# Kernel optimization log

Hardware: AMD Instinct MI355X
Metric: run time of the kernel (lower is better)

Reference implementation:

```python
import jax, jax.numpy as jnp
import numpy as np

B, S, D, H = 2, 2048, 1024, 16
HD = D // H  # head_dim = 64
ROPE_BASE = 10000.0
NEG_MIN = jnp.finfo(jnp.float32).min


def _rope_cos_sin(seq_len, head_dim):
    inv_freq = 1.0 / (ROPE_BASE ** (jnp.arange(0, head_dim, 2, dtype=jnp.float32) / head_dim))
    t = jnp.arange(seq_len, dtype=jnp.float32)
    freqs = jnp.einsum('i,j->ij', t, inv_freq)           # [S, HD/2]
    emb = jnp.concatenate([freqs, freqs], axis=-1)        # [S, HD]
    return jnp.cos(emb), jnp.sin(emb)


def _rotate_half(x):
    x1, x2 = jnp.split(x, 2, axis=-1)
    return jnp.concatenate([-x2, x1], axis=-1)


def setup_inputs() -> dict:
    key = jax.random.key(0)
    ks = jax.random.split(key, 5)
    sc = 0.02
    hidden_states = jax.random.normal(ks[0], (B, S, D), dtype=jnp.float32)
    wq = jax.random.normal(ks[1], (D, D), dtype=jnp.float32) * sc
    wk = jax.random.normal(ks[2], (D, D), dtype=jnp.float32) * sc
    wv = jax.random.normal(ks[3], (D, D), dtype=jnp.float32) * sc
    wo = jax.random.normal(ks[4], (D, D), dtype=jnp.float32) * sc
    # additive causal mask [B,1,S,S]: 0 on/below diagonal, large negative above
    causal = jnp.tril(jnp.ones((S, S), dtype=jnp.bool_))
    attention_mask = jnp.where(causal, 0.0, NEG_MIN)[None, None, :, :].astype(jnp.float32)
    attention_mask = jnp.broadcast_to(attention_mask, (B, 1, S, S))
    position_ids = jnp.broadcast_to(jnp.arange(S, dtype=jnp.int32)[None, :], (B, S))
    return {"hidden_states": hidden_states, "attention_mask": attention_mask,
            "wq": wq, "wk": wk, "wv": wv, "wo": wo, "position_ids": position_ids}


def reference(hidden_states, attention_mask, wq, wk, wv, wo, position_ids):
    bsz, q_len, _ = hidden_states.shape

    def shape_heads(x):
        return x.reshape(bsz, q_len, H, HD).transpose(0, 2, 1, 3)  # [B,H,S,HD]

    q = shape_heads(hidden_states @ wq)
    k = shape_heads(hidden_states @ wk)
    v = shape_heads(hidden_states @ wv)

    cos, sin = _rope_cos_sin(q_len, HD)                   # [S, HD]
    cos = cos[position_ids][:, None, :, :]                # [B,1,S,HD]
    sin = sin[position_ids][:, None, :, :]
    q = q * cos + _rotate_half(q) * sin
    k = k * cos + _rotate_half(k) * sin

    scores = jnp.einsum('bhqd,bhkd->bhqk', q, k) / jnp.sqrt(jnp.float32(HD))
    scores = jnp.maximum(scores + attention_mask, NEG_MIN)
    attn = jax.nn.softmax(scores, axis=-1)
    out = jnp.einsum('bhqk,bhkd->bhqd', attn, v)          # [B,H,S,HD]
    out = out.transpose(0, 2, 1, 3).reshape(bsz, q_len, D)
    return out @ wo
```

## Files before the change

### kernel.cpp

```cpp
#include <hip/hip_runtime.h>
#include <hip/hip_bf16.h>

#define B_ 2
#define S_ 2048
#define D_ 1024
#define H_ 16
#define HD_ 64

typedef unsigned short u16;
typedef __attribute__((ext_vector_type(8))) short short8;
typedef __attribute__((ext_vector_type(4))) float f32x4;

#if __has_builtin(__builtin_amdgcn_exp2f)
#define EXP2F(x) __builtin_amdgcn_exp2f(x)
#else
#define EXP2F(x) exp2f(x)
#endif

__device__ __forceinline__ u16 f2bf(float f) {
  union { float f; unsigned u; } v; v.f = f;
  unsigned r = v.u + 0x7fffu + ((v.u >> 16) & 1u);
  return (u16)(r >> 16);
}
__device__ __forceinline__ unsigned pkbf(float a, float b) {
  union { __hip_bfloat162 h; unsigned u; } v;
  v.h = __float22bfloat162_rn(float2{a, b});
  return v.u;
}
__device__ __forceinline__ void gload_lds16(const u16* g, u16* l) {
  __builtin_amdgcn_global_load_lds((const __attribute__((address_space(1))) void*)g,
                                   (__attribute__((address_space(3))) void*)l, 16, 0, 0);
}

template <int N> struct IC { static constexpr int v = N; };

__global__ __launch_bounds__(256) void prep_kernel(const float* __restrict__ hs,
                                                   const float* __restrict__ W0,
                                                   const float* __restrict__ W1,
                                                   const float* __restrict__ W2,
                                                   const float* __restrict__ W3,
                                                   u16* __restrict__ Xb,
                                                   u16* __restrict__ WT) {
  __shared__ float T[64][65];
  if (blockIdx.z == 4) {
    const int base = (blockIdx.y * 16 + blockIdx.x) * 4096 + threadIdx.x;
#pragma unroll 4
    for (int i = 0; i < 16; ++i) {
      const int idx = base + i * 256;
      const float4 v = ((const float4*)hs)[idx];
      ushort4 o;
      o.x = f2bf(v.x); o.y = f2bf(v.y); o.z = f2bf(v.z); o.w = f2bf(v.w);
      ((ushort4*)Xb)[idx] = o;
    }
    return;
  }
  const float* Wz[4] = {W0, W1, W2, W3};
  const float* W = Wz[blockIdx.z];
  u16* dst = WT + (size_t)blockIdx.z * (1024 * 1024);
  const int nb = blockIdx.x * 64, kb = blockIdx.y * 64;
  const int t = threadIdx.x;
  const int r = t >> 2, c4 = (t & 3) * 16;
#pragma unroll
  for (int i = 0; i < 4; ++i) {
    float4 v = *(const float4*)&W[(kb + r) * D_ + nb + c4 + i * 4];
    T[r][c4 + i * 4 + 0] = v.x;
    T[r][c4 + i * 4 + 1] = v.y;
    T[r][c4 + i * 4 + 2] = v.z;
    T[r][c4 + i * 4 + 3] = v.w;
  }
  __syncthreads();
#pragma unroll
  for (int i = 0; i < 4; ++i) {
    ushort4 o;
    o.x = f2bf(T[c4 + i * 4 + 0][r]);
    o.y = f2bf(T[c4 + i * 4 + 1][r]);
    o.z = f2bf(T[c4 + i * 4 + 2][r]);
    o.w = f2bf(T[c4 + i * 4 + 3][r]);
    *(ushort4*)&dst[(nb + r) * D_ + kb + c4 + i * 4] = o;
  }
}

template <int BN, int MODE>
__global__ __launch_bounds__(256) void gemm_kernel(const u16* __restrict__ A,
                                                   const u16* __restrict__ BT,
                                                   float* __restrict__ out0,
                                                   u16* __restrict__ oQ,
                                                   u16* __restrict__ oK,
                                                   u16* __restrict__ oV,
                                                   const int* __restrict__ posarr) {
  constexpr int K = D_;
  constexpr int BK = 32;
  constexpr int NSTEP = K / BK;
  constexpr int NT = BN / 32;
  constexpr int NBR = (BN * BK) / 2048;
  constexpr int ABANK = 128 * BK;
  constexpr int BBANK = BN * BK;
  constexpr int BUFSZ = ABANK + BBANK;
  constexpr int EPIU = (MODE == 1) ? 128 * 136 : 0;
  constexpr int SMU = (3 * BUFSZ > EPIU) ? 3 * BUFSZ : EPIU;
  __shared__ u16 smem[SMU];

  const int t = threadIdx.x, lane = t & 63, w = t >> 6;
  const int l15 = lane & 15, quad = lane >> 4;
  const int flat = blockIdx.x;
  const int xcd = flat & 7, j = flat >> 3;
  const int m0 = ((xcd << 2) + (j & 3)) * 128;
  const int n0 = (j >> 2) * BN;
  const int wm = (w >> 1) * 64, wn = (w & 1) * (BN / 2);

  f32x4 acc[4][NT];
#pragma unroll
  for (int mt = 0; mt < 4; ++mt)
#pragma unroll
    for (int nt = 0; nt < NT; ++nt) acc[mt][nt] = (f32x4){0.f, 0.f, 0.f, 0.f};

  const u16* agp[2]; int adst[2];
  const u16* bgp[NBR]; int bdst[NBR];
#pragma unroll
  for (int jj = 0; jj < 2; ++jj) {
    const int slot = jj * 256 + w * 64 + lane;
    const int row = slot >> 2, c = slot & 3, q = c ^ ((row >> 1) & 3);
    agp[jj] = A + (size_t)(m0 + row) * K + q * 8;
    adst[jj] = (jj * 256 + w * 64) * 8;
  }
#pragma unroll
  for (int jj = 0; jj < NBR; ++jj) {
    const int slot = jj * 256 + w * 64 + lane;
    const int row = slot >> 2, c = slot & 3, q = c ^ ((row >> 1) & 3);
    bgp[jj] = BT + (size_t)(n0 + row) * K + q * 8;
    bdst[jj] = ABANK + (jj * 256 + w * 64) * 8;
  }

  auto stage = [&](int k0, int buf) {
    u16* base = smem + buf * BUFSZ;
#pragma unroll
    for (int jj = 0; jj < 2; ++jj) gload_lds16(agp[jj] + k0, base + adst[jj]);
#pragma unroll
    for (int jj = 0; jj < NBR; ++jj) gload_lds16(bgp[jj] + k0, base + bdst[jj]);
  };

  int afo[4], bfo[NT];
#pragma unroll
  for (int mt = 0; mt < 4; ++mt) {
    const int row = wm + mt * 16 + l15;
    afo[mt] = row * BK + (quad ^ ((row >> 1) & 3)) * 8;
  }
#pragma unroll
  for (int nt = 0; nt < NT; ++nt) {
    const int col = wn + nt * 16 + l15;
    bfo[nt] = ABANK + col * BK + (quad ^ ((col >> 1) & 3)) * 8;
  }

  auto compute = [&](int buf) {
    const u16* base = smem + buf * BUFSZ;
    short8 af[4], bf[NT];
#pragma unroll
    for (int mt = 0; mt < 4; ++mt) af[mt] = *(const short8*)&base[afo[mt]];
#pragma unroll
    for (int nt = 0; nt < NT; ++nt) bf[nt] = *(const short8*)&base[bfo[nt]];
#pragma unroll
    for (int mt = 0; mt < 4; ++mt)
#pragma unroll
      for (int nt = 0; nt < NT; ++nt)
        acc[mt][nt] = __builtin_amdgcn_mfma_f32_16x16x32_bf16(af[mt], bf[nt], acc[mt][nt], 0, 0, 0);
  };

  stage(0, 0);
  stage(BK, 1);
  int bc = 0, bs = 2;
#pragma unroll 1
  for (int it = 0; it < NSTEP - 2; ++it) {
    if constexpr (MODE == 1) asm volatile("s_waitcnt vmcnt(4)" ::: "memory");
    else                     asm volatile("s_waitcnt vmcnt(3)" ::: "memory");
    __builtin_amdgcn_s_barrier();
    __builtin_amdgcn_sched_barrier(0);
    stage((it + 2) * BK, bs);
    compute(bc);
    bc = bc == 2 ? 0 : bc + 1;
    bs = bs == 2 ? 0 : bs + 1;
  }
  if constexpr (MODE == 1) asm volatile("s_waitcnt vmcnt(4)" ::: "memory");
  else                     asm volatile("s_waitcnt vmcnt(3)" ::: "memory");
  __builtin_amdgcn_s_barrier();
  __builtin_amdgcn_sched_barrier(0);
  compute(bc);
  bc = bc == 2 ? 0 : bc + 1;
  asm volatile("s_waitcnt vmcnt(0)" ::: "memory");
  __builtin_amdgcn_s_barrier();
  __builtin_amdgcn_sched_barrier(0);
  compute(bc);

  if (MODE == 0) {
#pragma unroll
    for (int mt = 0; mt < 4; ++mt) {
      const int row0 = m0 + wm + mt * 16 + quad * 4;
#pragma unroll
      for (int nt = 0; nt < NT; ++nt) {
        const int col = n0 + wn + nt * 16 + l15;
#pragma unroll
        for (int r = 0; r < 4; ++r) out0[(size_t)(row0 + r) * 1024 + col] = acc[mt][nt][r];
      }
    }
  } else {
    const int widx = n0 >> 10;
    if (widx == 2) {
      __syncthreads();
      u16* Epi = smem;
#pragma unroll
      for (int nt = 0; nt < NT; ++nt) {
        const int col = wn + nt * 16 + l15;
#pragma unroll
        for (int mt = 0; mt < 4; ++mt) {
          const int row0 = wm + mt * 16 + quad * 4;
          uint2 pk;
          pk.x = pkbf(acc[mt][nt][0], acc[mt][nt][1]);
          pk.y = pkbf(acc[mt][nt][2], acc[mt][nt][3]);
          *(uint2*)&Epi[col * 136 + row0] = pk;
        }
      }
      __syncthreads();
      const int col = t >> 1, half = t & 1;
      const int cc = (n0 + col) & 1023;
      const int h = cc >> 6, d = cc & 63;
      const int bb = m0 >> 11;
      const int s0 = (m0 & (S_ - 1)) + half * 64;
      u16* gp = oV + ((((size_t)(bb * H_ + h) * HD_ + d)) << 11) + s0;
#pragma unroll
      for (int i = 0; i < 8; ++i)
        ((uint4*)gp)[i] = *(const uint4*)&Epi[col * 136 + half * 64 + i * 8];
    } else {
      u16* dst = (widx == 0) ? oQ : oK;
      const float scale = (widx == 0) ? 0.18033688011f : 1.0f;
      float invf[2];
      invf[0] = exp2f(-0.41524101186f * (float)l15);
      invf[1] = exp2f(-0.41524101186f * (float)(16 + l15));
      __syncthreads();
      u16* Epi = smem;
#pragma unroll
      for (int mt = 0; mt < 4; ++mt) {
        const int lrow0 = wm + mt * 16 + quad * 4;
#pragma unroll
        for (int r = 0; r < 4; ++r) {
          const int rw = m0 + lrow0 + r;
          const int b = rw >> 11, s = rw & (S_ - 1);
          const float pos = (float)posarr[b * S_ + s];
#pragma unroll
          for (int nt2 = 0; nt2 < 2; ++nt2) {
            float sn, c;
            __sincosf(pos * invf[nt2], &sn, &c);
            const float x1 = acc[mt][nt2][r], x2 = acc[mt][nt2 + 2][r];
            const int d = nt2 * 16 + l15;
            Epi[(lrow0 + r) * 136 + wn + d] = f2bf((x1 * c - x2 * sn) * scale);
            Epi[(lrow0 + r) * 136 + wn + d + 32] = f2bf((x2 * c + x1 * sn) * scale);
          }
        }
      }
      __syncthreads();
      const int bb = m0 >> 11, s0 = m0 & (S_ - 1);
      const int sl = t >> 1, d0 = (t & 1) * 32;
#pragma unroll
      for (int hh = 0; hh < 2; ++hh) {
        const int h = ((n0 + hh * 64) & 1023) >> 6;
        u16* gp = dst + (((size_t)(bb * H_ + h) * S_ + s0 + sl) << 6) + d0;
#pragma unroll
        for (int k2 = 0; k2 < 4; ++k2)
          ((uint4*)gp)[k2] = *(const uint4*)&Epi[sl * 136 + hh * 64 + d0 + k2 * 8];
      }
    }
  }
}

__global__ __launch_bounds__(256, 2) void attn_kernel(const u16* __restrict__ Q,
                                                      const u16* __restrict__ Kx,
                                                      const u16* __restrict__ Vt,
                                                      u16* __restrict__ AO) {
  __shared__ u16 Ks[2][2][512 * 8];
  __shared__ u16 Vs[2][2][512 * 8];
  __shared__ u16 Pw[4][2][128 * 8];
  const int t = threadIdx.x;
  const int lane = t & 63, w = t >> 6;
  const int l15 = lane & 15, quad = lane >> 4;
  const int idx = blockIdx.x;
  const int pr = (idx >> 3) & 15;
  const int bh = (idx & 7) | ((idx >> 7) << 3);
  const int qtA = pr, qtB = 31 - pr;
  const u16* qp = Q + bh * (S_ * HD_);
  const u16* kp = Kx + bh * (S_ * HD_);
  const u16* vp = Vt + bh * (HD_ * S_);
  const int wq16 = w * 16;
  const int q_loA = qtA * 64 + wq16;
  const int q_loB = qtB * 64 + wq16;

  int srow[2], sq[2];
#pragma unroll
  for (int jj = 0; jj < 2; ++jj) {
    int slot = w * 128 + jj * 64 + lane;
    srow[jj] = slot >> 3;
    sq[jj] = (slot & 7) ^ (srow[jj] & 7);
  }
  auto stageT = [&](int kt, int buf, int tt) {
#pragma unroll
    for (int jj = 0; jj < 2; ++jj)
      gload_lds16(kp + (size_t)(kt * 64 + srow[jj]) * 64 + sq[jj] * 8,
                  &Ks[buf][tt][(w * 128 + jj * 64) * 8]);
#pragma unroll
    for (int jj = 0; jj < 2; ++jj)
      gload_lds16(vp + (size_t)srow[jj] * S_ + kt * 64 + sq[jj] * 8,
                  &Vs[buf][tt][(w * 128 + jj * 64) * 8]);
  };
  auto stageGroup = [&](int g, int buf, int ktmax) {
    const int kt0 = g * 2;
    stageT(kt0, buf, 0);
    if (kt0 + 1 <= ktmax) stageT(kt0 + 1, buf, 1);
  };

  short8 qfA[2], qfB[2];
#pragma unroll
  for (int kc = 0; kc < 2; ++kc) {
    qfA[kc] = *(const short8*)&qp[(q_loA + l15) * HD_ + kc * 32 + quad * 8];
    qfB[kc] = *(const short8*)&qp[(q_loB + l15) * HD_ + kc * 32 + quad * 8];
  }

  f32x4 oA[4], oB[4];
  f32x4 lsA = (f32x4){0.f, 0.f, 0.f, 0.f}, lsB = (f32x4){0.f, 0.f, 0.f, 0.f};
  float mA = -INFINITY, mB = -INFINITY;
#pragma unroll
  for (int i = 0; i < 4; ++i) {
    oA[i] = (f32x4){0.f, 0.f, 0.f, 0.f};
    oB[i] = (f32x4){0.f, 0.f, 0.f, 0.f};
  }
  const short8 ones = {0x3F80, 0x3F80, 0x3F80, 0x3F80, 0x3F80, 0x3F80, 0x3F80, 0x3F80};

  auto fusedStep = [&](auto NTT, int kt0, int qt_, const short8* qf,
                       f32x4* o, float& m_, f32x4& ls, int buf) {
    constexpr int N2 = decltype(NTT)::v;
    short8 kf[N2][8];
#pragma unroll
    for (int tt = 0; tt < N2; ++tt)
#pragma unroll
      for (int kc = 0; kc < 2; ++kc)
#pragma unroll
        for (int nt = 0; nt < 4; ++nt) {
          const int row = nt * 16 + l15;
          kf[tt][kc * 4 + nt] =
              *(const short8*)&Ks[buf][tt][(row * 8 + ((kc * 4 + quad) ^ (row & 7))) * 8];
        }
    f32x4 sa[N2 * 4];
#pragma unroll
    for (int i = 0; i < N2 * 4; ++i) sa[i] = (f32x4){0.f, 0.f, 0.f, 0.f};
#pragma unroll
    for (int tt = 0; tt < N2; ++tt)
#pragma unroll
      for (int kc = 0; kc < 2; ++kc)
#pragma unroll
        for (int nt = 0; nt < 4; ++nt)
          sa[tt * 4 + nt] = __builtin_amdgcn_mfma_f32_16x16x32_bf16(
              kf[tt][kc * 4 + nt], qf[kc], sa[tt * 4 + nt], 0, 0, 0);
#pragma unroll
    for (int tt = 0; tt < N2; ++tt)
      if (kt0 + tt == qt_) {
#pragma unroll
        for (int nt = 0; nt < 4; ++nt)
#pragma unroll
          for (int r = 0; r < 4; ++r)
            if (nt * 16 + quad * 4 + r > wq16 + l15) sa[tt * 4 + nt][r] = -INFINITY;
      }
    float mx = -INFINITY;
#pragma unroll
    for (int i = 0; i < N2 * 4; ++i)
      mx = fmaxf(mx, fmaxf(fmaxf(sa[i][0], sa[i][1]), fmaxf(sa[i][2], sa[i][3])));
    mx = fmaxf(mx, __shfl_xor(mx, 16));
    mx = fmaxf(mx, __shfl_xor(mx, 32));
    if (!__all(mx <= m_)) {
      const float mn = fmaxf(m_, mx);
      const float alpha = EXP2F(m_ - mn);
      m_ = mn;
#pragma unroll
      for (int dt = 0; dt < 4; ++dt)
#pragma unroll
        for (int r = 0; r < 4; ++r) o[dt][r] *= alpha;
      ls *= alpha;
    }
#pragma unroll
    for (int tt = 0; tt < N2; ++tt)
#pragma unroll
      for (int nt = 0; nt < 4; ++nt) {
        const int q = nt * 2 + (quad >> 1);
        uint2 pk;
        pk.x = pkbf(EXP2F(sa[tt * 4 + nt][0] - m_), EXP2F(sa[tt * 4 + nt][1] - m_));
        pk.y = pkbf(EXP2F(sa[tt * 4 + nt][2] - m_), EXP2F(sa[tt * 4 + nt][3] - m_));
        *(uint2*)&Pw[w][tt][(l15 * 8 + (q ^ (l15 & 7))) * 8 + (quad & 1) * 4] = pk;
      }
    short8 vf[N2][8];
#pragma unroll
    for (int tt = 0; tt < N2; ++tt)
#pragma unroll
      for (int dt = 0; dt < 4; ++dt)
#pragma unroll
        for (int kc = 0; kc < 2; ++kc) {
          const int row = dt * 16 + l15;
          vf[tt][dt * 2 + kc] =
              *(const short8*)&Vs[buf][tt][(row * 8 + ((kc * 4 + quad) ^ (row & 7))) * 8];
        }
#pragma unroll
    for (int tt = 0; tt < N2; ++tt)
#pragma unroll
      for (int kc = 0; kc < 2; ++kc) {
        short8 pf =
            *(const short8*)&Pw[w][tt][(l15 * 8 + (((kc * 4) + quad) ^ (l15 & 7))) * 8];
#pragma unroll
        for (int dt = 0; dt < 4; ++dt)
          o[dt] = __builtin_amdgcn_mfma_f32_16x16x32_bf16(vf[tt][dt * 2 + kc], pf, o[dt], 0, 0, 0);
        ls = __builtin_amdgcn_mfma_f32_16x16x32_bf16(ones, pf, ls, 0, 0, 0);
      }
  };

  const int ktmax = qtB;
  const int ngroups = (ktmax + 2) >> 1;
  stageGroup(0, 0, ktmax);
#pragma unroll 1
  for (int g = 0; g < ngroups; ++g) {
    __syncthreads();
    if (g + 1 < ngroups) stageGroup(g + 1, (g + 1) & 1, ktmax);
    const int buf = g & 1;
    const int kt0 = 2 * g;
    if (kt0 + 1 <= qtB) fusedStep(IC<2>{}, kt0, qtB, qfB, oB, mB, lsB, buf);
    else                fusedStep(IC<1>{}, kt0, qtB, qfB, oB, mB, lsB, buf);
    if (kt0 <= qtA) {
      if (kt0 + 1 <= qtA) fusedStep(IC<2>{}, kt0, qtA, qfA, oA, mA, lsA, buf);
      else                fusedStep(IC<1>{}, kt0, qtA, qfA, oA, mA, lsA, buf);
    }
  }

  const int b = bh >> 4, h = bh & 15;
  const float liA = 1.0f / lsA[0], liB = 1.0f / lsB[0];
  const size_t baseA = ((size_t)(b * S_ + q_loA + l15)) * D_ + h * HD_;
  const size_t baseB = ((size_t)(b * S_ + q_loB + l15)) * D_ + h * HD_;
#pragma unroll
  for (int dt = 0; dt < 4; ++dt)
#pragma unroll
    for (int rr = 0; rr < 2; ++rr) {
      *(unsigned*)&AO[baseA + dt * 16 + quad * 4 + rr * 2] =
          pkbf(oA[dt][rr * 2] * liA, oA[dt][rr * 2 + 1] * liA);
      *(unsigned*)&AO[baseB + dt * 16 + quad * 4 + rr * 2] =
          pkbf(oB[dt][rr * 2] * liB, oB[dt][rr * 2 + 1] * liB);
    }
}

extern "C" void kernel_launch(void* const* d_in, const int* in_sizes, int n_in,
                              void* d_out, int out_size, void* d_ws, size_t ws_size,
                              hipStream_t stream) {
  const float* hs = (const float*)d_in[0];
  const float* wq = (const float*)d_in[2];
  const float* wk = (const float*)d_in[3];
  const float* wv = (const float*)d_in[4];
  const float* wo = (const float*)d_in[5];
  const int* pos = (const int*)d_in[6];
  float* out = (float*)d_out;

  char* ws = (char*)d_ws;
  const size_t MB = (size_t)1 << 20;
  u16* Xb = (u16*)(ws);
  u16* WT = (u16*)(ws + 8 * MB);
  u16* Qh = (u16*)(ws + 16 * MB);
  u16* Kh = (u16*)(ws + 24 * MB);
  u16* Vt = (u16*)(ws + 32 * MB);
  u16* AO = (u16*)(ws + 40 * MB);

  prep_kernel<<<dim3(16, 16, 5), 256, 0, stream>>>(hs, wq, wk, wv, wo, Xb, WT);

  gemm_kernel<128, 1><<<768, 256, 0, stream>>>(Xb, WT, nullptr, Qh, Kh, Vt, pos);

  attn_kernel<<<512, 256, 0, stream>>>(Qh, Kh, Vt, AO);

  gemm_kernel<64, 0><<<512, 256, 0, stream>>>(AO, WT + 3 * 1024 * 1024, out,
                                              nullptr, nullptr, nullptr, nullptr);
}
```

Baseline: 204.4 us.

## Load K/V fragments directly from global memory, dropping LDS staging and barriers

Removes the double-buffered LDS staging of K and V tiles and the per-group __syncthreads. Each wave now loads its K and V MFMA fragments straight from global memory into registers. The loop is also reordered so both query tiles' QK^T run first, sharing the K fragments, before softmax and PV. This gets rid of barrier stalls and LDS traffic, but every wave now reads the same K/V data separately, giving four times the global/L2 traffic per block. It also loses the asynchronous prefetch overlap and raises register pressure.

```diff
diff --git a/kernel.cpp b/kernel.cpp
--- a/kernel.cpp
+++ b/kernel.cpp
@@ -274,8 +274,6 @@
                                                       const u16* __restrict__ Kx,
                                                       const u16* __restrict__ Vt,
                                                       u16* __restrict__ AO) {
-  __shared__ u16 Ks[2][2][512 * 8];
-  __shared__ u16 Vs[2][2][512 * 8];
   __shared__ u16 Pw[4][2][128 * 8];
   const int t = threadIdx.x;
   const int lane = t & 63, w = t >> 6;
@@ -291,29 +289,6 @@
   const int q_loA = qtA * 64 + wq16;
   const int q_loB = qtB * 64 + wq16;
 
-  int srow[2], sq[2];
-#pragma unroll
-  for (int jj = 0; jj < 2; ++jj) {
-    int slot = w * 128 + jj * 64 + lane;
-    srow[jj] = slot >> 3;
-    sq[jj] = (slot & 7) ^ (srow[jj] & 7);
-  }
-  auto stageT = [&](int kt, int buf, int tt) {
-#pragma unroll
-    for (int jj = 0; jj < 2; ++jj)
-      gload_lds16(kp + (size_t)(kt * 64 + srow[jj]) * 64 + sq[jj] * 8,
-                  &Ks[buf][tt][(w * 128 + jj * 64) * 8]);
-#pragma unroll
-    for (int jj = 0; jj < 2; ++jj)
-      gload_lds16(vp + (size_t)srow[jj] * S_ + kt * 64 + sq[jj] * 8,
-                  &Vs[buf][tt][(w * 128 + jj * 64) * 8]);
-  };
-  auto stageGroup = [&](int g, int buf, int ktmax) {
-    const int kt0 = g * 2;
-    stageT(kt0, buf, 0);
-    if (kt0 + 1 <= ktmax) stageT(kt0 + 1, buf, 1);
-  };
-
   short8 qfA[2], qfB[2];
 #pragma unroll
   for (int kc = 0; kc < 2; ++kc) {
@@ -331,21 +306,30 @@
   }
   const short8 ones = {0x3F80, 0x3F80, 0x3F80, 0x3F80, 0x3F80, 0x3F80, 0x3F80, 0x3F80};
 
-  auto fusedStep = [&](auto NTT, int kt0, int qt_, const short8* qf,
-                       f32x4* o, float& m_, f32x4& ls, int buf) {
-    constexpr int N2 = decltype(NTT)::v;
-    short8 kf[N2][8];
+  auto loadK = [&](auto TT, int kt0, short8 (*kfp)[8]) {
+    constexpr int N2 = decltype(TT)::v;
 #pragma unroll
     for (int tt = 0; tt < N2; ++tt)
 #pragma unroll
       for (int kc = 0; kc < 2; ++kc)
 #pragma unroll
-        for (int nt = 0; nt < 4; ++nt) {
-          const int row = nt * 16 + l15;
-          kf[tt][kc * 4 + nt] =
-              *(const short8*)&Ks[buf][tt][(row * 8 + ((kc * 4 + quad) ^ (row & 7))) * 8];
-        }
-    f32x4 sa[N2 * 4];
+        for (int nt = 0; nt < 4; ++nt)
+          kfp[tt][kc * 4 + nt] = *(const short8*)&kp[(size_t)((kt0 + tt) * 64 + nt * 16 + l15) * HD_ +
+                                                    (kc * 4 + quad) * 8];
+  };
+  auto loadV = [&](auto TT, int kt0, short8 (*vfp)[8]) {
+    constexpr int N2 = decltype(TT)::v;
+#pragma unroll
+    for (int tt = 0; tt < N2; ++tt)
+#pragma unroll
+      for (int dt = 0; dt < 4; ++dt)
+#pragma unroll
+        for (int kc = 0; kc < 2; ++kc)
+          vfp[tt][dt * 2 + kc] = *(const short8*)&vp[(size_t)(dt * 16 + l15) * S_ + (kt0 + tt) * 64 +
+                                                     (kc * 4 + quad) * 8];
+  };
+  auto qkPart = [&](auto TT, const short8* qf, const short8 (*kfp)[8], f32x4* sa) {
+    constexpr int N2 = decltype(TT)::v;
 #pragma unroll
     for (int i = 0; i < N2 * 4; ++i) sa[i] = (f32x4){0.f, 0.f, 0.f, 0.f};
 #pragma unroll
@@ -355,7 +339,11 @@
 #pragma unroll
         for (int nt = 0; nt < 4; ++nt)
           sa[tt * 4 + nt] = __builtin_amdgcn_mfma_f32_16x16x32_bf16(
-              kf[tt][kc * 4 + nt], qf[kc], sa[tt * 4 + nt], 0, 0, 0);
+              kfp[tt][kc * 4 + nt], qf[kc], sa[tt * 4 + nt], 0, 0, 0);
+  };
+  auto smPv = [&](auto TT, int kt0, int qt_, f32x4* sa, const short8 (*vfp)[8],
+                  f32x4* o, float& m_, f32x4& ls) {
+    constexpr int N2 = decltype(TT)::v;
 #pragma unroll
     for (int tt = 0; tt < N2; ++tt)
       if (kt0 + tt == qt_) {
@@ -391,44 +379,40 @@
         pk.y = pkbf(EXP2F(sa[tt * 4 + nt][2] - m_), EXP2F(sa[tt * 4 + nt][3] - m_));
         *(uint2*)&Pw[w][tt][(l15 * 8 + (q ^ (l15 & 7))) * 8 + (quad & 1) * 4] = pk;
       }
-    short8 vf[N2][8];
-#pragma unroll
-    for (int tt = 0; tt < N2; ++tt)
-#pragma unroll
-      for (int dt = 0; dt < 4; ++dt)
-#pragma unroll
-        for (int kc = 0; kc < 2; ++kc) {
-          const int row = dt * 16 + l15;
-          vf[tt][dt * 2 + kc] =
-              *(const short8*)&Vs[buf][tt][(row * 8 + ((kc * 4 + quad) ^ (row & 7))) * 8];
-        }
 #pragma unroll
     for (int tt = 0; tt < N2; ++tt)
 #pragma unroll
       for (int kc = 0; kc < 2; ++kc) {
-        short8 pf =
-            *(const short8*)&Pw[w][tt][(l15 * 8 + (((kc * 4) + quad) ^ (l15 & 7))) * 8];
+        short8 pf = *(const short8*)&Pw[w][tt][(l15 * 8 + (((kc * 4) + quad) ^ (l15 & 7))) * 8];
 #pragma unroll
         for (int dt = 0; dt < 4; ++dt)
-          o[dt] = __builtin_amdgcn_mfma_f32_16x16x32_bf16(vf[tt][dt * 2 + kc], pf, o[dt], 0, 0, 0);
+          o[dt] = __builtin_amdgcn_mfma_f32_16x16x32_bf16(vfp[tt][dt * 2 + kc], pf, o[dt], 0, 0, 0);
         ls = __builtin_amdgcn_mfma_f32_16x16x32_bf16(ones, pf, ls, 0, 0, 0);
       }
   };
 
-  const int ktmax = qtB;
-  const int ngroups = (ktmax + 2) >> 1;
-  stageGroup(0, 0, ktmax);
+  const int ngroups = (qtB + 2) >> 1;
 #pragma unroll 1
   for (int g = 0; g < ngroups; ++g) {
-    __syncthreads();
-    if (g + 1 < ngroups) stageGroup(g + 1, (g + 1) & 1, ktmax);
-    const int buf = g & 1;
     const int kt0 = 2 * g;
-    if (kt0 + 1 <= qtB) fusedStep(IC<2>{}, kt0, qtB, qfB, oB, mB, lsB, buf);
-    else                fusedStep(IC<1>{}, kt0, qtB, qfB, oB, mB, lsB, buf);
-    if (kt0 <= qtA) {
-      if (kt0 + 1 <= qtA) fusedStep(IC<2>{}, kt0, qtA, qfA, oA, mA, lsA, buf);
-      else                fusedStep(IC<1>{}, kt0, qtA, qfA, oA, mA, lsA, buf);
+    short8 kf[2][8], vf[2][8];
+    if (kt0 + 1 <= qtB) {
+      loadK(IC<2>{}, kt0, kf);
+      f32x4 saB[8], saA[8];
+      qkPart(IC<2>{}, qfB, kf, saB);
+      const int tA = (kt0 > qtA) ? 0 : ((kt0 + 1 <= qtA) ? 2 : 1);
+      if (tA == 2)      qkPart(IC<2>{}, qfA, kf, saA);
+      else if (tA == 1) qkPart(IC<1>{}, qfA, kf, saA);
+      loadV(IC<2>{}, kt0, vf);
+      smPv(IC<2>{}, kt0, qtB, saB, vf, oB, mB, lsB);
+      if (tA == 2)      smPv(IC<2>{}, kt0, qtA, saA, vf, oA, mA, lsA);
+      else if (tA == 1) smPv(IC<1>{}, kt0, qtA, saA, vf, oA, mA, lsA);
+    } else {
+      loadK(IC<1>{}, kt0, kf);
+      f32x4 saB[4];
+      qkPart(IC<1>{}, qfB, kf, saB);
+      loadV(IC<1>{}, kt0, vf);
+      smPv(IC<1>{}, kt0, qtB, saB, vf, oB, mB, lsB);
     }
   }
 
```

New measurement: 276.6 us. +35.3%, slower.

## Share K/V LDS fragments across both query tiles in attention loop

Applied to the files above, without the earlier changes.

Splits the fused attention step into separate K load, QK MFMA, V load and softmax+PV phases. The main loop loads the K and V fragments from LDS once per group and reuses them for both query tiles, which previously reloaded them independently. The aim is to halve LDS reads for K/V and interleave the two tiles' QK work. In exchange it raises register pressure by keeping two score arrays and both fragment sets live, which may lower occupancy or cause spills.

```diff
diff --git a/kernel.cpp b/kernel.cpp
--- a/kernel.cpp
+++ b/kernel.cpp
@@ -331,10 +331,8 @@
   }
   const short8 ones = {0x3F80, 0x3F80, 0x3F80, 0x3F80, 0x3F80, 0x3F80, 0x3F80, 0x3F80};
 
-  auto fusedStep = [&](auto NTT, int kt0, int qt_, const short8* qf,
-                       f32x4* o, float& m_, f32x4& ls, int buf) {
-    constexpr int N2 = decltype(NTT)::v;
-    short8 kf[N2][8];
+  auto loadKls = [&](auto TT, int buf, short8 (*kfp)[8]) {
+    constexpr int N2 = decltype(TT)::v;
 #pragma unroll
     for (int tt = 0; tt < N2; ++tt)
 #pragma unroll
@@ -342,10 +340,25 @@
 #pragma unroll
         for (int nt = 0; nt < 4; ++nt) {
           const int row = nt * 16 + l15;
-          kf[tt][kc * 4 + nt] =
+          kfp[tt][kc * 4 + nt] =
               *(const short8*)&Ks[buf][tt][(row * 8 + ((kc * 4 + quad) ^ (row & 7))) * 8];
         }
-    f32x4 sa[N2 * 4];
+  };
+  auto loadVls = [&](auto TT, int buf, short8 (*vfp)[8]) {
+    constexpr int N2 = decltype(TT)::v;
+#pragma unroll
+    for (int tt = 0; tt < N2; ++tt)
+#pragma unroll
+      for (int dt = 0; dt < 4; ++dt)
+#pragma unroll
+        for (int kc = 0; kc < 2; ++kc) {
+          const int row = dt * 16 + l15;
+          vfp[tt][dt * 2 + kc] =
+              *(const short8*)&Vs[buf][tt][(row * 8 + ((kc * 4 + quad) ^ (row & 7))) * 8];
+        }
+  };
+  auto qkPart = [&](auto TT, const short8* qf, const short8 (*kfp)[8], f32x4* sa) {
+    constexpr int N2 = decltype(TT)::v;
 #pragma unroll
     for (int i = 0; i < N2 * 4; ++i) sa[i] = (f32x4){0.f, 0.f, 0.f, 0.f};
 #pragma unroll
@@ -355,7 +368,11 @@
 #pragma unroll
         for (int nt = 0; nt < 4; ++nt)
           sa[tt * 4 + nt] = __builtin_amdgcn_mfma_f32_16x16x32_bf16(
-              kf[tt][kc * 4 + nt], qf[kc], sa[tt * 4 + nt], 0, 0, 0);
+              kfp[tt][kc * 4 + nt], qf[kc], sa[tt * 4 + nt], 0, 0, 0);
+  };
+  auto smPv = [&](auto TT, int kt0, int qt_, f32x4* sa, const short8 (*vfp)[8],
+                  f32x4* o, float& m_, f32x4& ls) {
+    constexpr int N2 = decltype(TT)::v;
 #pragma unroll
     for (int tt = 0; tt < N2; ++tt)
       if (kt0 + tt == qt_) {
@@ -391,26 +408,14 @@
         pk.y = pkbf(EXP2F(sa[tt * 4 + nt][2] - m_), EXP2F(sa[tt * 4 + nt][3] - m_));
         *(uint2*)&Pw[w][tt][(l15 * 8 + (q ^ (l15 & 7))) * 8 + (quad & 1) * 4] = pk;
       }
-    short8 vf[N2][8];
-#pragma unroll
-    for (int tt = 0; tt < N2; ++tt)
-#pragma unroll
-      for (int dt = 0; dt < 4; ++dt)
-#pragma unroll
-        for (int kc = 0; kc < 2; ++kc) {
-          const int row = dt * 16 + l15;
-          vf[tt][dt * 2 + kc] =
-              *(const short8*)&Vs[buf][tt][(row * 8 + ((kc * 4 + quad) ^ (row & 7))) * 8];
-        }
 #pragma unroll
     for (int tt = 0; tt < N2; ++tt)
 #pragma unroll
       for (int kc = 0; kc < 2; ++kc) {
-        short8 pf =
-            *(const short8*)&Pw[w][tt][(l15 * 8 + (((kc * 4) + quad) ^ (l15 & 7))) * 8];
+        short8 pf = *(const short8*)&Pw[w][tt][(l15 * 8 + (((kc * 4) + quad) ^ (l15 & 7))) * 8];
 #pragma unroll
         for (int dt = 0; dt < 4; ++dt)
-          o[dt] = __builtin_amdgcn_mfma_f32_16x16x32_bf16(vf[tt][dt * 2 + kc], pf, o[dt], 0, 0, 0);
+          o[dt] = __builtin_amdgcn_mfma_f32_16x16x32_bf16(vfp[tt][dt * 2 + kc], pf, o[dt], 0, 0, 0);
         ls = __builtin_amdgcn_mfma_f32_16x16x32_bf16(ones, pf, ls, 0, 0, 0);
       }
   };
@@ -424,11 +429,23 @@
     if (g + 1 < ngroups) stageGroup(g + 1, (g + 1) & 1, ktmax);
     const int buf = g & 1;
     const int kt0 = 2 * g;
-    if (kt0 + 1 <= qtB) fusedStep(IC<2>{}, kt0, qtB, qfB, oB, mB, lsB, buf);
-    else                fusedStep(IC<1>{}, kt0, qtB, qfB, oB, mB, lsB, buf);
-    if (kt0 <= qtA) {
-      if (kt0 + 1 <= qtA) fusedStep(IC<2>{}, kt0, qtA, qfA, oA, mA, lsA, buf);
-      else                fusedStep(IC<1>{}, kt0, qtA, qfA, oA, mA, lsA, buf);
+    short8 kf[2][8], vf[2][8];
+    f32x4 saB[8], saA[8];
+    if (kt0 + 1 <= qtB) {
+      loadKls(IC<2>{}, buf, kf);
+      qkPart(IC<2>{}, qfB, kf, saB);
+      const int tA = (kt0 > qtA) ? 0 : ((kt0 + 1 <= qtA) ? 2 : 1);
+      if (tA == 2)      qkPart(IC<2>{}, qfA, kf, saA);
+      else if (tA == 1) qkPart(IC<1>{}, qfA, kf, saA);
+      loadVls(IC<2>{}, buf, vf);
+      smPv(IC<2>{}, kt0, qtB, saB, vf, oB, mB, lsB);
+      if (tA == 2)      smPv(IC<2>{}, kt0, qtA, saA, vf, oA, mA, lsA);
+      else if (tA == 1) smPv(IC<1>{}, kt0, qtA, saA, vf, oA, mA, lsA);
+    } else {
+      loadKls(IC<1>{}, buf, kf);
+      qkPart(IC<1>{}, qfB, kf, saB);
+      loadVls(IC<1>{}, buf, vf);
+      smPv(IC<1>{}, kt0, qtB, saB, vf, oB, mB, lsB);
     }
   }
 
```

Result: no change. 206.8 us (+1.2%).
